# Kernel optimization log

Hardware: AMD Instinct MI355X
Metric: run time of the kernel (lower is better)

The kernel has to match this reference:

```python
import jax, jax.numpy as jnp
import numpy as np

T, B, DIM, N_STATE = 2048, 16, 1024, 1024
EPS = 1e-6


def setup_inputs() -> dict:
    key = jax.random.key(0)
    kx, kk, kv, kq = jax.random.split(key, 4)
    xavier = np.sqrt(2.0 / (N_STATE + DIM)).astype(np.float32)
    return {
        "x": jax.random.normal(kx, (T, B, DIM), dtype=jnp.float32),
        "W_k": jax.random.normal(kk, (N_STATE, DIM), dtype=jnp.float32) * xavier,
        "W_v": jax.random.normal(kv, (N_STATE, DIM), dtype=jnp.float32) * xavier,
        "W_q": jax.random.normal(kq, (N_STATE, DIM), dtype=jnp.float32) * xavier,
    }


def reference(x, W_k, W_v, W_q):
    # Projections for all timesteps at once: [T, B, n]
    k = jnp.einsum("tbd,nd->tbn", x, W_k)
    v = jnp.einsum("tbd,nd->tbn", x, W_v)
    q = jnp.einsum("tbd,nd->tbn", x, W_q)
    # L2-normalize k per (t, b) over the state dim (matches k_t.norm(dim=-1))
    k_norm = k / (jnp.linalg.norm(k, axis=-1, keepdims=True) + EPS)

    Tn, Bn, n = k.shape
    S0 = jnp.zeros((Bn, n), dtype=x.dtype)

    def step(S, inp):
        k_t, v_t, q_t = inp
        # Delta update with OUTPUT gating + tanh nonlinearity
        S_new = jnp.tanh(S * (1.0 - k_t * k_t) + v_t * k_t)
        Sq = S_new * q_t
        out = Sq * jax.nn.silu(Sq)
        return S_new, out

    S_final, output = jax.lax.scan(step, S0, (k_norm, v, q))
    return output, S_final
```

## Files before the change

### kernel.cpp

```cpp
#include <hip/hip_runtime.h>
#include <hip/hip_fp16.h>

#define T_STEPS 2048
#define BATCH 16
#define DIMD 1024
#define NSTATE 1024
#define MROWS (T_STEPS * BATCH)
#define NCH (BATCH * NSTATE)

typedef _Float16 f16x8 __attribute__((ext_vector_type(8)));
typedef float f32x4 __attribute__((ext_vector_type(4)));

#define GAS(p) ((const __attribute__((address_space(1))) void*)(p))
#define LAS(p) ((__attribute__((address_space(3))) void*)(p))

__global__ void cvt_kernel(const float* __restrict__ src, _Float16* __restrict__ dst, int n8) {
  int i = blockIdx.x * blockDim.x + threadIdx.x;
  if (i >= n8) return;
  const float4* s4 = (const float4*)src;
  float4 a = s4[(size_t)i * 2];
  float4 b = s4[(size_t)i * 2 + 1];
  f16x8 o;
  o[0] = (_Float16)a.x; o[1] = (_Float16)a.y; o[2] = (_Float16)a.z; o[3] = (_Float16)a.w;
  o[4] = (_Float16)b.x; o[5] = (_Float16)b.y; o[6] = (_Float16)b.z; o[7] = (_Float16)b.w;
  *((f16x8*)dst + i) = o;
}

__global__ void cvtW_kernel(const float* __restrict__ wk, const float* __restrict__ wv,
                            const float* __restrict__ wq, _Float16* __restrict__ dst) {
  const float* src = blockIdx.y == 0 ? wk : blockIdx.y == 1 ? wv : wq;
  int i = blockIdx.x * blockDim.x + threadIdx.x;
  const float4* s4 = (const float4*)src;
  float4 a = s4[(size_t)i * 2];
  float4 b = s4[(size_t)i * 2 + 1];
  f16x8 o;
  o[0] = (_Float16)a.x; o[1] = (_Float16)a.y; o[2] = (_Float16)a.z; o[3] = (_Float16)a.w;
  o[4] = (_Float16)b.x; o[5] = (_Float16)b.y; o[6] = (_Float16)b.z; o[7] = (_Float16)b.w;
  *((f16x8*)dst + (size_t)blockIdx.y * (NSTATE * DIMD / 8) + i) = o;
}

__global__ __launch_bounds__(512, 1) void gemm_kernel(const _Float16* __restrict__ A,
                                                      const _Float16* __restrict__ Wcat,
                                                      _Float16* __restrict__ KVQt,
                                                      float* __restrict__ rnpart) {
  __shared__ _Float16 lds[65536];
  const int tid = threadIdx.x;
  const int lane = tid & 63;
  const int w = tid >> 6;
  const int wm = w >> 2;
  const int wn = w & 3;

  const int bid = blockIdx.x;
  const int swz = (bid & 7) * 192 + (bid >> 3);
  const int mat = swz >> 9;
  const int rem = swz & 511;
  const int tileM = rem >> 2;
  const int tileN = rem & 3;

  const _Float16* Ag = A + (size_t)tileM * 256 * DIMD;
  const _Float16* Bg = Wcat + (size_t)mat * NSTATE * DIMD + (size_t)tileN * 256 * DIMD;

  const int s0 = tid, s1 = tid + 512;
  const int sr0 = s0 >> 2, sc0 = ((s0 & 3) ^ ((s0 >> 3) & 3)) * 8;
  const int sr1 = s1 >> 2, sc1 = ((s1 & 3) ^ ((s1 >> 3) & 3)) * 8;

#define STAGE_H(G, buf, hb, TT, h)                                                      \
  do {                                                                                  \
    __builtin_amdgcn_global_load_lds(                                                   \
        GAS(G + (size_t)sr0 * DIMD + (TT) * 64 + (h) * 32 + sc0),                       \
        LAS(lds + (buf) * 32768 + ((hb) + (h)) * 8192 + s0 * 8), 16, 0, 0);             \
    __builtin_amdgcn_global_load_lds(                                                   \
        GAS(G + (size_t)sr1 * DIMD + (TT) * 64 + (h) * 32 + sc1),                       \
        LAS(lds + (buf) * 32768 + ((hb) + (h)) * 8192 + s1 * 8), 16, 0, 0);             \
  } while (0)

  f32x4 acc[8][4];
#pragma unroll
  for (int m = 0; m < 8; ++m)
#pragma unroll
    for (int n = 0; n < 4; ++n)
      acc[m][n] = (f32x4){0.f, 0.f, 0.f, 0.f};

  STAGE_H(Ag, 0, 0, 0, 0);
  STAGE_H(Bg, 0, 2, 0, 0);
  STAGE_H(Ag, 0, 0, 0, 1);
  STAGE_H(Bg, 0, 2, 0, 1);

  const int fr = lane & 15;
  const int cbp = ((lane >> 4) ^ ((fr >> 1) & 3)) * 8;

#define KTILE(T)                                                                        \
  do {                                                                                  \
    const int buf = (T) & 1, bufn = buf ^ 1;                                            \
    f16x8 a0[8], b0[4], a1[8], b1[4];                                                   \
                    \
    asm volatile("s_waitcnt vmcnt(4)" ::: "memory");                                    \
    __builtin_amdgcn_s_barrier();                                                       \
    __builtin_amdgcn_sched_barrier(0);                                                  \
    if ((T) + 1 < 16) STAGE_H(Ag, bufn, 0, (T) + 1, 0);                                 \
    _Pragma("unroll") for (int m = 0; m < 8; ++m)                                       \
        a0[m] = *(const f16x8*)(lds + buf * 32768 + 0 * 8192 +                          \
                                (wm * 128 + m * 16 + fr) * 32 + cbp);                   \
    _Pragma("unroll") for (int n = 0; n < 4; ++n)                                       \
        b0[n] = *(const f16x8*)(lds + buf * 32768 + 2 * 8192 +                          \
                                (wn * 64 + n * 16 + fr) * 32 + cbp);                    \
    __builtin_amdgcn_s_setprio(1);                                                      \
    _Pragma("unroll") for (int m = 0; m < 8; ++m) _Pragma("unroll") for (int n = 0; n < 2; ++n) \
        acc[m][n] = __builtin_amdgcn_mfma_f32_16x16x32_f16(a0[m], b0[n], acc[m][n], 0, 0, 0); \
    __builtin_amdgcn_s_setprio(0);                                                      \
                                         \
    if ((T) + 1 < 16) STAGE_H(Bg, bufn, 2, (T) + 1, 0);                                 \
    __builtin_amdgcn_s_setprio(1);                                                      \
    _Pragma("unroll") for (int m = 0; m < 8; ++m) _Pragma("unroll") for (int n = 2; n < 4; ++n) \
        acc[m][n] = __builtin_amdgcn_mfma_f32_16x16x32_f16(a0[m], b0[n], acc[m][n], 0, 0, 0); \
    __builtin_amdgcn_s_setprio(0);                                                      \
                    \
    if ((T) + 1 < 16) {                                                                 \
      asm volatile("s_waitcnt vmcnt(4)" ::: "memory");                                  \
    } else {                                                                            \
      asm volatile("s_waitcnt vmcnt(0)" ::: "memory");                                  \
    }                                                                                   \
    __builtin_amdgcn_s_barrier();                                                       \
    __builtin_amdgcn_sched_barrier(0);                                                  \
    if ((T) + 1 < 16) STAGE_H(Ag, bufn, 0, (T) + 1, 1);                                 \
    _Pragma("unroll") for (int m = 0; m < 8; ++m)                                       \
        a1[m] = *(const f16x8*)(lds + buf * 32768 + 1 * 8192 +                          \
                                (wm * 128 + m * 16 + fr) * 32 + cbp);                   \
    _Pragma("unroll") for (int n = 0; n < 4; ++n)                                       \
        b1[n] = *(const f16x8*)(lds + buf * 32768 + 3 * 8192 +                          \
                                (wn * 64 + n * 16 + fr) * 32 + cbp);                    \
    __builtin_amdgcn_s_setprio(1);                                                      \
    _Pragma("unroll") for (int m = 0; m < 8; ++m) _Pragma("unroll") for (int n = 0; n < 2; ++n) \
        acc[m][n] = __builtin_amdgcn_mfma_f32_16x16x32_f16(a1[m], b1[n], acc[m][n], 0, 0, 0); \
    __builtin_amdgcn_s_setprio(0);                                                      \
                                         \
    if ((T) + 1 < 16) STAGE_H(Bg, bufn, 2, (T) + 1, 1);                                 \
    __builtin_amdgcn_s_setprio(1);                                                      \
    _Pragma("unroll") for (int m = 0; m < 8; ++m) _Pragma("unroll") for (int n = 2; n < 4; ++n) \
        acc[m][n] = __builtin_amdgcn_mfma_f32_16x16x32_f16(a1[m], b1[n], acc[m][n], 0, 0, 0); \
    __builtin_amdgcn_s_setprio(0);                                                      \
  } while (0)

  KTILE(0);  KTILE(1);  KTILE(2);  KTILE(3);
  KTILE(4);  KTILE(5);  KTILE(6);  KTILE(7);
  KTILE(8);  KTILE(9);  KTILE(10); KTILE(11);
  KTILE(12); KTILE(13); KTILE(14); KTILE(15);

  const int cc = lane & 15;
  const int l4 = lane >> 4;
  _Float16* Cb = KVQt + (size_t)mat * ((size_t)MROWS * NSTATE) +
                 (size_t)(tileM * 2 + wm) * ((size_t)NCH * 8);
#pragma unroll
  for (int n = 0; n < 4; ++n)
#pragma unroll
    for (int j = 0; j < 4; ++j) {
      f16x8 pk;
#pragma unroll
      for (int m = 0; m < 8; ++m) pk[m] = (_Float16)acc[m][n][j];
      const int b = l4 * 4 + j;
      const int gcol = tileN * 256 + wn * 64 + n * 16 + cc;
      *(f16x8*)(Cb + ((size_t)(b * 1024 + gcol)) * 8) = pk;
    }

  if (mat == 0) {
#pragma unroll
    for (int m = 0; m < 8; ++m)
#pragma unroll
      for (int j = 0; j < 4; ++j) {
        float p = 0.f;
#pragma unroll
        for (int n = 0; n < 4; ++n) p += acc[m][n][j] * acc[m][n][j];
        p += __shfl_xor(p, 1);
        p += __shfl_xor(p, 2);
        p += __shfl_xor(p, 4);
        p += __shfl_xor(p, 8);
        if (cc == 0) {
          const int gr = tileM * 256 + wm * 128 + m * 16 + l4 * 4 + j;
          rnpart[(size_t)(tileN * 4 + wn) * MROWS + gr] = p;
        }
      }
  }
}

__global__ void rnfin_kernel(const float* __restrict__ part, float* __restrict__ rnT) {
  const int r = blockIdx.x * 256 + threadIdx.x;
  float s = 0.f;
#pragma unroll
  for (int i = 0; i < 16; ++i) s += part[(size_t)i * MROWS + r];
  rnT[(r & 15) * T_STEPS + (r >> 4)] = 1.f / (sqrtf(s) + 1e-6f);
}

#define STILE 16

#define LOADT(P, t0in)                                                        \
  do {                                                                        \
    const int tc = ((t0in) < T_STEPS) ? (t0in) : (T_STEPS - STILE);           \
    const size_t o0 = ((size_t)(tc >> 3) * NCH + c) * 8;                      \
    P##k0 = *(const f16x8*)(Kt + o0);                                         \
    P##k1 = *(const f16x8*)(Kt + o0 + (size_t)NCH * 8);                       \
    P##v0 = *(const f16x8*)(Vt + o0);                                         \
    P##v1 = *(const f16x8*)(Vt + o0 + (size_t)NCH * 8);                       \
    P##q0 = *(const f16x8*)(Qt + o0);                                         \
    P##q1 = *(const f16x8*)(Qt + o0 + (size_t)NCH * 8);                       \
    P##r0 = *(const f32x4*)(rnT + bb + tc);                                   \
    P##r1 = *(const f32x4*)(rnT + bb + tc + 4);                               \
    P##r2 = *(const f32x4*)(rnT + bb + tc + 8);                               \
    P##r3 = *(const f32x4*)(rnT + bb + tc + 12);                              \
  } while (0)

#define STEPT(P, t0)                                                          \
  do {                                                                        \
    float a2[STILE], b2[STILE], qf[STILE];                                    \
    _Pragma("unroll") for (int i = 0; i < STILE; ++i) {                       \
      float kf = (float)((i < 8) ? P##k0[i & 7] : P##k1[i & 7]);              \
      float vf = (float)((i < 8) ? P##v0[i & 7] : P##v1[i & 7]);              \
      float rv = (i < 4) ? P##r0[i & 3]                                       \
               : (i < 8) ? P##r1[i & 3]                                       \
               : (i < 12) ? P##r2[i & 3] : P##r3[i & 3];                      \
      float kn = kf * rv;                                                     \
      a2[i] = L2E2 - (L2E2 * kn) * kn;                                        \
      b2[i] = L2E2 * (vf * kn);                                               \
      qf[i] = (float)((i < 8) ? P##q0[i & 7] : P##q1[i & 7]);                 \
    }                                                                         \
    _Pragma("unroll") for (int i = 0; i < STILE; ++i) {                       \
      float u = fmaf(S, a2[i], b2[i]);                                        \
      float e = __builtin_amdgcn_exp2f(u);                                    \
      float r = __builtin_amdgcn_rcpf(e + 1.f);                               \
      S = fmaf(-2.f, r, 1.f);                                                 \
      float z = S * qf[i];                                                    \
      float sg = __builtin_amdgcn_rcpf(1.f + __builtin_amdgcn_exp2f(-L2E * z)); \
      out[(size_t)((t0) + i) * NCH + c] = z * z * sg;                         \
    }                                                                         \
  } while (0)

__global__ __launch_bounds__(64) void scan_kernel(const _Float16* __restrict__ Kt,
                                                  const _Float16* __restrict__ Vt,
                                                  const _Float16* __restrict__ Qt,
                                                  const float* __restrict__ rnT,
                                                  float* __restrict__ out,
                                                  float* __restrict__ sfin) {
  const int c = blockIdx.x * 64 + threadIdx.x;
  const int bb = (c >> 10) * T_STEPS;
  constexpr float L2E2 = 2.8853900817779268f;
  constexpr float L2E = 1.4426950408889634f;
  float S = 0.f;
  f16x8 Ak0, Ak1, Av0, Av1, Aq0, Aq1;
  f16x8 Bk0, Bk1, Bv0, Bv1, Bq0, Bq1;
  f32x4 Ar0, Ar1, Ar2, Ar3, Br0, Br1, Br2, Br3;

  LOADT(A, 0);
  for (int t0 = 0; t0 < T_STEPS; t0 += 2 * STILE) {
    LOADT(B, t0 + STILE);
    STEPT(A, t0);
    LOADT(A, t0 + 2 * STILE);
    STEPT(B, t0 + STILE);
  }
  sfin[c] = S;
}

extern "C" void kernel_launch(void* const* d_in, const int* in_sizes, int n_in,
                              void* d_out, int out_size, void* d_ws, size_t ws_size,
                              hipStream_t stream) {
  const float* x = (const float*)d_in[0];
  const float* Wk = (const float*)d_in[1];
  const float* Wv = (const float*)d_in[2];
  const float* Wq = (const float*)d_in[3];

  char* ws = (char*)d_ws;
  _Float16* xh = (_Float16*)ws;
  _Float16* Wh = (_Float16*)(ws + 67108864ull);
  _Float16* KVQt = (_Float16*)(ws + 67108864ull + 6291456ull);
  float* rnpart = (float*)(ws + 67108864ull + 6291456ull + 201326592ull);
  float* rnT = (float*)(ws + 67108864ull + 6291456ull + 201326592ull + 2097152ull);

  int n8x = MROWS * DIMD / 8;
  cvt_kernel<<<(n8x + 255) / 256, 256, 0, stream>>>(x, xh, n8x);
  cvtW_kernel<<<dim3(NSTATE * DIMD / 8 / 256, 3), 256, 0, stream>>>(Wk, Wv, Wq, Wh);

  gemm_kernel<<<1536, 512, 0, stream>>>(xh, Wh, KVQt, rnpart);

  rnfin_kernel<<<MROWS / 256, 256, 0, stream>>>(rnpart, rnT);

  const _Float16* Kt = KVQt;
  const _Float16* Vt = KVQt + (size_t)MROWS * NSTATE;
  const _Float16* Qt = KVQt + 2ull * MROWS * NSTATE;
  float* outp = (float*)d_out;
  scan_kernel<<<NCH / 64, 64, 0, stream>>>(Kt, Vt, Qt, rnT, outp, outp + (size_t)MROWS * NSTATE);
}
```

Before: 431.8 us.

## Split GEMM fragment loads into half-tiles and triple-buffer scan prefetch

The projection GEMM now loads only four A fragments at a time and issues each half of the M tile as a separate MFMA block. Each block has its own explicit lgkmcnt wait and workgroup barriers, which lowers register pressure at the cost of more synchronisation. LDS staging now uses explicit region indices. The recurrent scan kernel moves from double-buffered to triple-buffered register prefetch of the K/V/Q/rnorm tiles, with a two-tile epilogue, to hide more global-load latency on the serial time loop. Both changes add registers or barriers in exchange for latency hiding.

```diff
diff --git a/kernel.cpp b/kernel.cpp
--- a/kernel.cpp
+++ b/kernel.cpp
@@ -64,14 +64,14 @@
   const int sr0 = s0 >> 2, sc0 = ((s0 & 3) ^ ((s0 >> 3) & 3)) * 8;
   const int sr1 = s1 >> 2, sc1 = ((s1 & 3) ^ ((s1 >> 3) & 3)) * 8;
 
-#define STAGE_H(G, buf, hb, TT, h)                                                      \
+#define STAGE_H(G, buf, reg, TT, h)                                                     \
   do {                                                                                  \
     __builtin_amdgcn_global_load_lds(                                                   \
         GAS(G + (size_t)sr0 * DIMD + (TT) * 64 + (h) * 32 + sc0),                       \
-        LAS(lds + (buf) * 32768 + ((hb) + (h)) * 8192 + s0 * 8), 16, 0, 0);             \
+        LAS(lds + (buf) * 32768 + (reg) * 8192 + s0 * 8), 16, 0, 0);                    \
     __builtin_amdgcn_global_load_lds(                                                   \
         GAS(G + (size_t)sr1 * DIMD + (TT) * 64 + (h) * 32 + sc1),                       \
-        LAS(lds + (buf) * 32768 + ((hb) + (h)) * 8192 + s1 * 8), 16, 0, 0);             \
+        LAS(lds + (buf) * 32768 + (reg) * 8192 + s1 * 8), 16, 0, 0);                    \
   } while (0)
 
   f32x4 acc[8][4];
@@ -83,62 +83,75 @@
 
   STAGE_H(Ag, 0, 0, 0, 0);
   STAGE_H(Bg, 0, 2, 0, 0);
-  STAGE_H(Ag, 0, 0, 0, 1);
-  STAGE_H(Bg, 0, 2, 0, 1);
+  STAGE_H(Ag, 0, 1, 0, 1);
+  STAGE_H(Bg, 0, 3, 0, 1);
 
   const int fr = lane & 15;
   const int cbp = ((lane >> 4) ^ ((fr >> 1) & 3)) * 8;
+
+#define LDA(dst, region, mi)                                                            \
+  dst = *(const f16x8*)(lds + buf * 32768 + (region) * 8192 +                           \
+                        (wm * 128 + (mi) * 16 + fr) * 32 + cbp)
+#define LDB(dst, region, ni)                                                            \
+  dst = *(const f16x8*)(lds + buf * 32768 + (region) * 8192 +                           \
+                        (wn * 64 + (ni) * 16 + fr) * 32 + cbp)
 
 #define KTILE(T)                                                                        \
   do {                                                                                  \
     const int buf = (T) & 1, bufn = buf ^ 1;                                            \
-    f16x8 a0[8], b0[4], a1[8], b1[4];                                                   \
-                    \
+    f16x8 aF[4], bF[4];                                                                 \
+      \
     asm volatile("s_waitcnt vmcnt(4)" ::: "memory");                                    \
     __builtin_amdgcn_s_barrier();                                                       \
     __builtin_amdgcn_sched_barrier(0);                                                  \
-    if ((T) + 1 < 16) STAGE_H(Ag, bufn, 0, (T) + 1, 0);                                 \
-    _Pragma("unroll") for (int m = 0; m < 8; ++m)                                       \
-        a0[m] = *(const f16x8*)(lds + buf * 32768 + 0 * 8192 +                          \
-                                (wm * 128 + m * 16 + fr) * 32 + cbp);                   \
-    _Pragma("unroll") for (int n = 0; n < 4; ++n)                                       \
-        b0[n] = *(const f16x8*)(lds + buf * 32768 + 2 * 8192 +                          \
-                                (wn * 64 + n * 16 + fr) * 32 + cbp);                    \
+    if ((T) < 15) STAGE_H(Ag, bufn, 0, (T) + 1, 0);                                     \
+    _Pragma("unroll") for (int m = 0; m < 4; ++m) LDA(aF[m], 0, m);                     \
+    _Pragma("unroll") for (int n = 0; n < 4; ++n) LDB(bF[n], 2, n);                     \
+    asm volatile("s_waitcnt lgkmcnt(0)" ::: "memory");                                  \
+    __builtin_amdgcn_sched_barrier(0);                                                  \
     __builtin_amdgcn_s_setprio(1);                                                      \
-    _Pragma("unroll") for (int m = 0; m < 8; ++m) _Pragma("unroll") for (int n = 0; n < 2; ++n) \
-        acc[m][n] = __builtin_amdgcn_mfma_f32_16x16x32_f16(a0[m], b0[n], acc[m][n], 0, 0, 0); \
+    _Pragma("unroll") for (int m = 0; m < 4; ++m) _Pragma("unroll") for (int n = 0; n < 4; ++n) \
+        acc[m][n] = __builtin_amdgcn_mfma_f32_16x16x32_f16(aF[m], bF[n], acc[m][n], 0, 0, 0); \
     __builtin_amdgcn_s_setprio(0);                                                      \
-                                         \
-    if ((T) + 1 < 16) STAGE_H(Bg, bufn, 2, (T) + 1, 0);                                 \
+    __builtin_amdgcn_s_barrier();                                                       \
+                 \
+    if ((T) < 15) STAGE_H(Bg, bufn, 2, (T) + 1, 0);                                     \
+    _Pragma("unroll") for (int m = 0; m < 4; ++m) LDA(aF[m], 0, m + 4);                 \
+    asm volatile("s_waitcnt lgkmcnt(0)" ::: "memory");                                  \
+    __builtin_amdgcn_sched_barrier(0);                                                  \
     __builtin_amdgcn_s_setprio(1);                                                      \
-    _Pragma("unroll") for (int m = 0; m < 8; ++m) _Pragma("unroll") for (int n = 2; n < 4; ++n) \
-        acc[m][n] = __builtin_amdgcn_mfma_f32_16x16x32_f16(a0[m], b0[n], acc[m][n], 0, 0, 0); \
+    _Pragma("unroll") for (int m = 0; m < 4; ++m) _Pragma("unroll") for (int n = 0; n < 4; ++n) \
+        acc[m + 4][n] = __builtin_amdgcn_mfma_f32_16x16x32_f16(aF[m], bF[n], acc[m + 4][n], 0, 0, 0); \
     __builtin_amdgcn_s_setprio(0);                                                      \
-                    \
-    if ((T) + 1 < 16) {                                                                 \
+    __builtin_amdgcn_s_barrier();                                                       \
+      \
+    if ((T) < 15) {                                                                     \
       asm volatile("s_waitcnt vmcnt(4)" ::: "memory");                                  \
     } else {                                                                            \
       asm volatile("s_waitcnt vmcnt(0)" ::: "memory");                                  \
     }                                                                                   \
     __builtin_amdgcn_s_barrier();                                                       \
     __builtin_amdgcn_sched_barrier(0);                                                  \
-    if ((T) + 1 < 16) STAGE_H(Ag, bufn, 0, (T) + 1, 1);                                 \
-    _Pragma("unroll") for (int m = 0; m < 8; ++m)                                       \
-        a1[m] = *(const f16x8*)(lds + buf * 32768 + 1 * 8192 +                          \
-                                (wm * 128 + m * 16 + fr) * 32 + cbp);                   \
-    _Pragma("unroll") for (int n = 0; n < 4; ++n)                                       \
-        b1[n] = *(const f16x8*)(lds + buf * 32768 + 3 * 8192 +                          \
-                                (wn * 64 + n * 16 + fr) * 32 + cbp);                    \
+    if ((T) < 15) STAGE_H(Ag, bufn, 1, (T) + 1, 1);                                     \
+    _Pragma("unroll") for (int m = 0; m < 4; ++m) LDA(aF[m], 1, m);                     \
+    _Pragma("unroll") for (int n = 0; n < 4; ++n) LDB(bF[n], 3, n);                     \
+    asm volatile("s_waitcnt lgkmcnt(0)" ::: "memory");                                  \
+    __builtin_amdgcn_sched_barrier(0);                                                  \
     __builtin_amdgcn_s_setprio(1);                                                      \
-    _Pragma("unroll") for (int m = 0; m < 8; ++m) _Pragma("unroll") for (int n = 0; n < 2; ++n) \
-        acc[m][n] = __builtin_amdgcn_mfma_f32_16x16x32_f16(a1[m], b1[n], acc[m][n], 0, 0, 0); \
+    _Pragma("unroll") for (int m = 0; m < 4; ++m) _Pragma("unroll") for (int n = 0; n < 4; ++n) \
+        acc[m][n] = __builtin_amdgcn_mfma_f32_16x16x32_f16(aF[m], bF[n], acc[m][n], 0, 0, 0); \
     __builtin_amdgcn_s_setprio(0);                                                      \
-                                         \
-    if ((T) + 1 < 16) STAGE_H(Bg, bufn, 2, (T) + 1, 1);                                 \
+    __builtin_amdgcn_s_barrier();                                                       \
+                 \
+    if ((T) < 15) STAGE_H(Bg, bufn, 3, (T) + 1, 1);                                     \
+    _Pragma("unroll") for (int m = 0; m < 4; ++m) LDA(aF[m], 1, m + 4);                 \
+    asm volatile("s_waitcnt lgkmcnt(0)" ::: "memory");                                  \
+    __builtin_amdgcn_sched_barrier(0);                                                  \
     __builtin_amdgcn_s_setprio(1);                                                      \
-    _Pragma("unroll") for (int m = 0; m < 8; ++m) _Pragma("unroll") for (int n = 2; n < 4; ++n) \
-        acc[m][n] = __builtin_amdgcn_mfma_f32_16x16x32_f16(a1[m], b1[n], acc[m][n], 0, 0, 0); \
+    _Pragma("unroll") for (int m = 0; m < 4; ++m) _Pragma("unroll") for (int n = 0; n < 4; ++n) \
+        acc[m + 4][n] = __builtin_amdgcn_mfma_f32_16x16x32_f16(aF[m], bF[n], acc[m + 4][n], 0, 0, 0); \
     __builtin_amdgcn_s_setprio(0);                                                      \
+    __builtin_amdgcn_s_barrier();                                                       \
   } while (0)
 
   KTILE(0);  KTILE(1);  KTILE(2);  KTILE(3);
@@ -246,15 +259,21 @@
   float S = 0.f;
   f16x8 Ak0, Ak1, Av0, Av1, Aq0, Aq1;
   f16x8 Bk0, Bk1, Bv0, Bv1, Bq0, Bq1;
-  f32x4 Ar0, Ar1, Ar2, Ar3, Br0, Br1, Br2, Br3;
+  f16x8 Ck0, Ck1, Cv0, Cv1, Cq0, Cq1;
+  f32x4 Ar0, Ar1, Ar2, Ar3, Br0, Br1, Br2, Br3, Cr0, Cr1, Cr2, Cr3;
 
   LOADT(A, 0);
-  for (int t0 = 0; t0 < T_STEPS; t0 += 2 * STILE) {
-    LOADT(B, t0 + STILE);
+  LOADT(B, STILE);
+  for (int t0 = 0; t0 + 3 * STILE <= T_STEPS; t0 += 3 * STILE) {
+    LOADT(C, t0 + 2 * STILE);
     STEPT(A, t0);
-    LOADT(A, t0 + 2 * STILE);
+    LOADT(A, t0 + 3 * STILE);
     STEPT(B, t0 + STILE);
+    LOADT(B, t0 + 4 * STILE);
+    STEPT(C, t0 + 2 * STILE);
   }
+  STEPT(A, T_STEPS - 2 * STILE);
+  STEPT(B, T_STEPS - STILE);
   sfin[c] = S;
 }
 
```

New measurement: 381.8 us. 11.6% less time.

## Split scan into state-only producer chain and chunked parallel output workers

Applied to the files above, without the earlier changes.

Replaces the single 256-block sequential scan with a fused kernel. 256 producer blocks run only the state recurrence, without q or silu, and publish the state every 128 steps into a buffer guarded by flags. 4096 consumer blocks each take one 128-step chunk, spin-wait on the flag for the previous chunk's state, and then compute the full outputs. This exposes far more parallelism for the output-heavy part. The risks are spin-wait deadlock if consumer blocks get scheduled ahead of producers, plus extra flag and state-buffer traffic. The GEMM staging macro is also reparameterized, with equivalent LDS offsets.

```diff
diff --git a/kernel.cpp b/kernel.cpp
--- a/kernel.cpp
+++ b/kernel.cpp
@@ -39,6 +39,10 @@
   *((f16x8*)dst + (size_t)blockIdx.y * (NSTATE * DIMD / 8) + i) = o;
 }
 
+__global__ void zeroflags_kernel(int* __restrict__ flags) {
+  flags[blockIdx.x * 256 + threadIdx.x] = 0;
+}
+
 __global__ __launch_bounds__(512, 1) void gemm_kernel(const _Float16* __restrict__ A,
                                                       const _Float16* __restrict__ Wcat,
                                                       _Float16* __restrict__ KVQt,
@@ -64,14 +68,14 @@
   const int sr0 = s0 >> 2, sc0 = ((s0 & 3) ^ ((s0 >> 3) & 3)) * 8;
   const int sr1 = s1 >> 2, sc1 = ((s1 & 3) ^ ((s1 >> 3) & 3)) * 8;
 
-#define STAGE_H(G, buf, hb, TT, h)                                                      \
+#define STAGE_H(G, buf, reg, TT, h)                                                     \
   do {                                                                                  \
     __builtin_amdgcn_global_load_lds(                                                   \
         GAS(G + (size_t)sr0 * DIMD + (TT) * 64 + (h) * 32 + sc0),                       \
-        LAS(lds + (buf) * 32768 + ((hb) + (h)) * 8192 + s0 * 8), 16, 0, 0);             \
+        LAS(lds + (buf) * 32768 + (reg) * 8192 + s0 * 8), 16, 0, 0);                    \
     __builtin_amdgcn_global_load_lds(                                                   \
         GAS(G + (size_t)sr1 * DIMD + (TT) * 64 + (h) * 32 + sc1),                       \
-        LAS(lds + (buf) * 32768 + ((hb) + (h)) * 8192 + s1 * 8), 16, 0, 0);             \
+        LAS(lds + (buf) * 32768 + (reg) * 8192 + s1 * 8), 16, 0, 0);                    \
   } while (0)
 
   f32x4 acc[8][4];
@@ -83,8 +87,8 @@
 
   STAGE_H(Ag, 0, 0, 0, 0);
   STAGE_H(Bg, 0, 2, 0, 0);
-  STAGE_H(Ag, 0, 0, 0, 1);
-  STAGE_H(Bg, 0, 2, 0, 1);
+  STAGE_H(Ag, 0, 1, 0, 1);
+  STAGE_H(Bg, 0, 3, 0, 1);
 
   const int fr = lane & 15;
   const int cbp = ((lane >> 4) ^ ((fr >> 1) & 3)) * 8;
@@ -93,7 +97,7 @@
   do {                                                                                  \
     const int buf = (T) & 1, bufn = buf ^ 1;                                            \
     f16x8 a0[8], b0[4], a1[8], b1[4];                                                   \
-                    \
+                 \
     asm volatile("s_waitcnt vmcnt(4)" ::: "memory");                                    \
     __builtin_amdgcn_s_barrier();                                                       \
     __builtin_amdgcn_sched_barrier(0);                                                  \
@@ -114,7 +118,7 @@
     _Pragma("unroll") for (int m = 0; m < 8; ++m) _Pragma("unroll") for (int n = 2; n < 4; ++n) \
         acc[m][n] = __builtin_amdgcn_mfma_f32_16x16x32_f16(a0[m], b0[n], acc[m][n], 0, 0, 0); \
     __builtin_amdgcn_s_setprio(0);                                                      \
-                    \
+                  \
     if ((T) + 1 < 16) {                                                                 \
       asm volatile("s_waitcnt vmcnt(4)" ::: "memory");                                  \
     } else {                                                                            \
@@ -122,7 +126,7 @@
     }                                                                                   \
     __builtin_amdgcn_s_barrier();                                                       \
     __builtin_amdgcn_sched_barrier(0);                                                  \
-    if ((T) + 1 < 16) STAGE_H(Ag, bufn, 0, (T) + 1, 1);                                 \
+    if ((T) + 1 < 16) STAGE_H(Ag, bufn, 1, (T) + 1, 1);                                 \
     _Pragma("unroll") for (int m = 0; m < 8; ++m)                                       \
         a1[m] = *(const f16x8*)(lds + buf * 32768 + 1 * 8192 +                          \
                                 (wm * 128 + m * 16 + fr) * 32 + cbp);                   \
@@ -134,7 +138,7 @@
         acc[m][n] = __builtin_amdgcn_mfma_f32_16x16x32_f16(a1[m], b1[n], acc[m][n], 0, 0, 0); \
     __builtin_amdgcn_s_setprio(0);                                                      \
                                          \
-    if ((T) + 1 < 16) STAGE_H(Bg, bufn, 2, (T) + 1, 1);                                 \
+    if ((T) + 1 < 16) STAGE_H(Bg, bufn, 3, (T) + 1, 1);                                 \
     __builtin_amdgcn_s_setprio(1);                                                      \
     _Pragma("unroll") for (int m = 0; m < 8; ++m) _Pragma("unroll") for (int n = 2; n < 4; ++n) \
         acc[m][n] = __builtin_amdgcn_mfma_f32_16x16x32_f16(a1[m], b1[n], acc[m][n], 0, 0, 0); \
@@ -191,6 +195,55 @@
 }
 
 #define STILE 16
+constexpr float L2E2c = 2.8853900817779268f;
+constexpr float L2Ec = 1.4426950408889634f;
+
+#define LOADP(P, t0in)                                                        \
+  do {                                                                        \
+    const int tc = ((t0in) < T_STEPS) ? (t0in) : (T_STEPS - STILE);           \
+    const size_t o0 = ((size_t)(tc >> 3) * NCH + c) * 8;                      \
+    P##k0 = *(const f16x8*)(Kt + o0);                                         \
+    P##k1 = *(const f16x8*)(Kt + o0 + (size_t)NCH * 8);                       \
+    P##v0 = *(const f16x8*)(Vt + o0);                                         \
+    P##v1 = *(const f16x8*)(Vt + o0 + (size_t)NCH * 8);                       \
+    P##r0 = *(const f32x4*)(rnT + bb + tc);                                   \
+    P##r1 = *(const f32x4*)(rnT + bb + tc + 4);                               \
+    P##r2 = *(const f32x4*)(rnT + bb + tc + 8);                               \
+    P##r3 = *(const f32x4*)(rnT + bb + tc + 12);                              \
+  } while (0)
+
+#define STEPP(P, t0)                                                          \
+  do {                                                                        \
+    float p2[STILE], m2[STILE];                                               \
+    _Pragma("unroll") for (int i = 0; i < STILE; ++i) {                       \
+      float kf = (float)((i < 8) ? P##k0[i & 7] : P##k1[i & 7]);              \
+      float vf = (float)((i < 8) ? P##v0[i & 7] : P##v1[i & 7]);              \
+      float rv = (i < 4) ? P##r0[i & 3]                                       \
+               : (i < 8) ? P##r1[i & 3]                                       \
+               : (i < 12) ? P##r2[i & 3] : P##r3[i & 3];                      \
+      float kn = kf * rv;                                                     \
+      float a2 = L2E2c - (L2E2c * kn) * kn;                                   \
+      float b2 = L2E2c * (vf * kn);                                           \
+      p2[i] = a2 + b2;                                                        \
+      m2[i] = -2.f * a2;                                                      \
+    }                                                                         \
+    _Pragma("unroll") for (int i = 0; i < STILE; ++i) {                       \
+      float u = fmaf(m2[i], r, p2[i]);                                        \
+      float e = __builtin_amdgcn_exp2f(u);                                    \
+      r = __builtin_amdgcn_rcpf(e + 1.f);                                     \
+    }                                                                         \
+    if ((((t0) + STILE) & 127) == 0) {                                        \
+      const int j = ((t0) + STILE) >> 7;                                      \
+      float Sv = fmaf(-2.f, r, 1.f);                                          \
+      if (j < 16) {                                                           \
+        Sb[(size_t)(j - 1) * NCH + c] = Sv;                                   \
+        __threadfence();                                                      \
+        if (threadIdx.x == 0) atomicExch(&flags[(j - 1) * 256 + cb], 1);      \
+      } else {                                                                \
+        sfin[c] = Sv;                                                         \
+      }                                                                       \
+    }                                                                         \
+  } while (0)
 
 #define LOADT(P, t0in)                                                        \
   do {                                                                        \
@@ -218,44 +271,83 @@
                : (i < 8) ? P##r1[i & 3]                                       \
                : (i < 12) ? P##r2[i & 3] : P##r3[i & 3];                      \
       float kn = kf * rv;                                                     \
-      a2[i] = L2E2 - (L2E2 * kn) * kn;                                        \
-      b2[i] = L2E2 * (vf * kn);                                               \
+      a2[i] = L2E2c - (L2E2c * kn) * kn;                                      \
+      b2[i] = L2E2c * (vf * kn);                                              \
       qf[i] = (float)((i < 8) ? P##q0[i & 7] : P##q1[i & 7]);                 \
     }                                                                         \
     _Pragma("unroll") for (int i = 0; i < STILE; ++i) {                       \
       float u = fmaf(S, a2[i], b2[i]);                                        \
       float e = __builtin_amdgcn_exp2f(u);                                    \
-      float r = __builtin_amdgcn_rcpf(e + 1.f);                               \
-      S = fmaf(-2.f, r, 1.f);                                                 \
+      float rr = __builtin_amdgcn_rcpf(e + 1.f);                              \
+      S = fmaf(-2.f, rr, 1.f);                                                \
       float z = S * qf[i];                                                    \
-      float sg = __builtin_amdgcn_rcpf(1.f + __builtin_amdgcn_exp2f(-L2E * z)); \
+      float sg = __builtin_amdgcn_rcpf(1.f + __builtin_amdgcn_exp2f(-L2Ec * z)); \
       out[(size_t)((t0) + i) * NCH + c] = z * z * sg;                         \
     }                                                                         \
   } while (0)
 
-__global__ __launch_bounds__(64) void scan_kernel(const _Float16* __restrict__ Kt,
-                                                  const _Float16* __restrict__ Vt,
-                                                  const _Float16* __restrict__ Qt,
-                                                  const float* __restrict__ rnT,
-                                                  float* __restrict__ out,
-                                                  float* __restrict__ sfin) {
-  const int c = blockIdx.x * 64 + threadIdx.x;
-  const int bb = (c >> 10) * T_STEPS;
-  constexpr float L2E2 = 2.8853900817779268f;
-  constexpr float L2E = 1.4426950408889634f;
-  float S = 0.f;
-  f16x8 Ak0, Ak1, Av0, Av1, Aq0, Aq1;
-  f16x8 Bk0, Bk1, Bv0, Bv1, Bq0, Bq1;
-  f32x4 Ar0, Ar1, Ar2, Ar3, Br0, Br1, Br2, Br3;
-
-  LOADT(A, 0);
-  for (int t0 = 0; t0 < T_STEPS; t0 += 2 * STILE) {
-    LOADT(B, t0 + STILE);
-    STEPT(A, t0);
-    LOADT(A, t0 + 2 * STILE);
-    STEPT(B, t0 + STILE);
+__global__ __launch_bounds__(64) void scan_fused_kernel(const _Float16* __restrict__ Kt,
+                                                        const _Float16* __restrict__ Vt,
+                                                        const _Float16* __restrict__ Qt,
+                                                        const float* __restrict__ rnT,
+                                                        float* __restrict__ Sb,
+                                                        int* __restrict__ flags,
+                                                        float* __restrict__ out,
+                                                        float* __restrict__ sfin) {
+  if (blockIdx.x < 256) {
+    const int cb = blockIdx.x;
+    const int c = cb * 64 + threadIdx.x;
+    const int bb = (c >> 10) * T_STEPS;
+    float r = 0.5f;
+    f16x8 Ak0, Ak1, Av0, Av1;
+    f16x8 Bk0, Bk1, Bv0, Bv1;
+    f16x8 Ck0, Ck1, Cv0, Cv1;
+    f32x4 Ar0, Ar1, Ar2, Ar3, Br0, Br1, Br2, Br3, Cr0, Cr1, Cr2, Cr3;
+
+    LOADP(A, 0);
+    LOADP(B, STILE);
+    for (int t0 = 0; t0 + 3 * STILE <= T_STEPS; t0 += 3 * STILE) {
+      LOADP(C, t0 + 2 * STILE);
+      STEPP(A, t0);
+      LOADP(A, t0 + 3 * STILE);
+      STEPP(B, t0 + STILE);
+      LOADP(B, t0 + 4 * STILE);
+      STEPP(C, t0 + 2 * STILE);
+    }
+    STEPP(A, T_STEPS - 2 * STILE);
+    STEPP(B, T_STEPS - STILE);
+  } else {
+    const int idx = blockIdx.x - 256;
+    const int chunk = idx >> 8;
+    const int cb = idx & 255;
+    const int c = cb * 64 + threadIdx.x;
+    const int bb = (c >> 10) * T_STEPS;
+    float S;
+    if (chunk == 0) {
+      S = 0.f;
+    } else {
+      if (threadIdx.x == 0) {
+        while (atomicAdd(&flags[(chunk - 1) * 256 + cb], 0) == 0)
+          __builtin_amdgcn_s_sleep(8);
+      }
+      __threadfence();
+      S = Sb[(size_t)(chunk - 1) * NCH + c];
+    }
+    const int base = chunk * 128;
+    f16x8 Ak0, Ak1, Av0, Av1, Aq0, Aq1;
+    f16x8 Bk0, Bk1, Bv0, Bv1, Bq0, Bq1;
+    f32x4 Ar0, Ar1, Ar2, Ar3, Br0, Br1, Br2, Br3;
+
+    LOADT(A, base);
+#pragma unroll
+    for (int tt = 0; tt < 4; ++tt) {
+      const int t = base + tt * 32;
+      LOADT(B, t + STILE);
+      STEPT(A, t);
+      LOADT(A, t + 2 * STILE);
+      STEPT(B, t + STILE);
+    }
   }
-  sfin[c] = S;
 }
 
 extern "C" void kernel_launch(void* const* d_in, const int* in_sizes, int n_in,
@@ -272,6 +364,10 @@
   _Float16* KVQt = (_Float16*)(ws + 67108864ull + 6291456ull);
   float* rnpart = (float*)(ws + 67108864ull + 6291456ull + 201326592ull);
   float* rnT = (float*)(ws + 67108864ull + 6291456ull + 201326592ull + 2097152ull);
+  float* Sb = (float*)(ws + 67108864ull + 6291456ull + 201326592ull + 2097152ull + 131072ull);
+  int* flags = (int*)(ws + 67108864ull + 6291456ull + 201326592ull + 2097152ull + 131072ull + 1048576ull);
+
+  zeroflags_kernel<<<15, 256, 0, stream>>>(flags);
 
   int n8x = MROWS * DIMD / 8;
   cvt_kernel<<<(n8x + 255) / 256, 256, 0, stream>>>(x, xh, n8x);
@@ -285,5 +381,7 @@
   const _Float16* Vt = KVQt + (size_t)MROWS * NSTATE;
   const _Float16* Qt = KVQt + 2ull * MROWS * NSTATE;
   float* outp = (float*)d_out;
-  scan_kernel<<<NCH / 64, 64, 0, stream>>>(Kt, Vt, Qt, rnT, outp, outp + (size_t)MROWS * NSTATE);
-}
+  float* sfin = outp + (size_t)MROWS * NSTATE;
+
+  scan_fused_kernel<<<256 + 4096, 64, 0, stream>>>(Kt, Vt, Qt, rnT, Sb, flags, outp, sfin);
+}
```

After: 673.3 us. +56.0%, slower.
